# Performance work log

Measured on AMD Instinct MI355X. Metric: run time of the kernel, lower is better.

The kernel has to match this reference:

```python
import jax, jax.numpy as jnp
import numpy as np

B, C, H, W = 4, 256, 48, 48
KD, NH, AR = 32, 8, 4
D = AR * KD            # 128, value dim per head
NHKD = NH * KD         # 256
DH = NH * D            # 1024
EPS = 1e-5


def _bn(y, g, b):
    # BN with fresh running stats (mean=0, var=1): y*g/sqrt(1+eps)+b, over channel dim
    s = g / jnp.sqrt(jnp.float32(1.0) + EPS)
    return y * s[None, :, None] + b[None, :, None]


def setup_inputs() -> dict:
    key = jax.random.key(0)
    ks = jax.random.split(key, 13)
    w = lambda k, sh: jax.random.normal(k, sh, jnp.float32) * 0.05
    g = lambda k, sh: 1.0 + jax.random.normal(k, sh, jnp.float32) * 0.05
    return {
        "x": jax.random.normal(ks[0], (B, C, H, W), jnp.float32),
        "wq": w(ks[1], (NHKD, C)), "gq": g(ks[2], (NHKD,)), "bq": w(ks[3], (NHKD,)),
        "wk": w(ks[4], (NHKD, C)), "gk": g(ks[5], (NHKD,)), "bk": w(ks[6], (NHKD,)),
        "wv": w(ks[7], (DH, C)),   "gv": g(ks[8], (DH,)),   "bv": w(ks[9], (DH,)),
        "wp": w(ks[10], (C, DH)),  "gp": g(ks[11], (C,)),   "bp": w(ks[12], (C,)),
    }


def reference(x, wq, gq, bq, wk, gk, bk, wv, gv, bv, wp, gp, bp):
    b, c, h, w = x.shape
    n = h * w
    xf = x.reshape(b, c, n)                                   # [B,C,N]
    # 1x1 conv == channel matmul, then BN
    q = _bn(jnp.einsum('oc,bcn->bon', wq, xf), gq, bq).reshape(b, NH, KD, n)
    k = _bn(jnp.einsum('oc,bcn->bon', wk, xf), gk, bk).reshape(b, NH, KD, n)
    v = _bn(jnp.einsum('oc,bcn->bon', wv, xf), gv, bv).reshape(b, NH, D, n)
    # NOTE: original forward does NOT apply self.scale
    attn = jax.nn.softmax(jnp.einsum('bhkn,bhkm->bhnm', q, k), axis=-1)  # [B,H,N,N]
    xx = jnp.einsum('bhnm,bhdm->bhdn', attn, v).reshape(b, DH, n)        # [B,DH,N]
    out = _bn(jnp.einsum('oc,bcn->bon', wp, jax.nn.relu(xx)), gp, bp)
    return out.reshape(b, c, h, w)
```

## Files before the change

### kernel.cpp

```cpp
#include <hip/hip_runtime.h>

#define BB 4
#define C 256
#define HW 2304
#define NH 8
#define KD 32
#define D 128
#define DH 1024
#define MQ 256

typedef unsigned short bf16u;
typedef __attribute__((ext_vector_type(8))) short short8;
typedef __attribute__((ext_vector_type(4))) short bfx4;
typedef __attribute__((ext_vector_type(4))) float f32x4;
typedef __attribute__((ext_vector_type(4))) unsigned ux4;
typedef __attribute__((ext_vector_type(2))) unsigned ux2;

union U8 { ux4 u; short8 s; };

__device__ __forceinline__ bf16u f2b(float f) {
    unsigned u = __float_as_uint(f);
    return (bf16u)((u + 0x7fffu + ((u >> 16) & 1u)) >> 16);
}
__device__ __forceinline__ unsigned pkb(float a, float b) {
    return __builtin_amdgcn_perm(__float_as_uint(b) + 0x8000u,
                                 __float_as_uint(a) + 0x8000u, 0x07060302u);
}

__device__ __forceinline__ void glds16(const bf16u* g, bf16u* l) {
    __builtin_amdgcn_global_load_lds(
        (const __attribute__((address_space(1))) unsigned int*)g,
        (__attribute__((address_space(3))) unsigned int*)l,
        16, 0, 0);
}

#define MFMA32 __builtin_amdgcn_mfma_f32_16x16x32_bf16

__global__ __launch_bounds__(256) void prep(
    const float* __restrict__ wq, const float* __restrict__ wk, const float* __restrict__ wv,
    const float* __restrict__ gq, const float* __restrict__ bq,
    const float* __restrict__ gk, const float* __restrict__ bk,
    const float* __restrict__ gv, const float* __restrict__ bv,
    bf16u* __restrict__ WcT, float* __restrict__ biasc)
{
    const float rs = rsqrtf(1.0f + 1e-5f);
    const float L2E = 1.4426950408889634f;
    const int t = threadIdx.x, blk = blockIdx.x;
    if (blk < 192) {
        const int idx = (blk*256 + t) * 8;
        const int row = idx >> 8;
        const int k   = idx & 255;
        const float* src; float sc;
        if (row < 256)      { src = wq + idx;            sc = gq[row]*rs*L2E; }
        else if (row < 512) { src = wk + (idx - 65536);  sc = gk[row-256]*rs; }
        else                { src = wv + (idx - 131072); sc = gv[row-512]*rs; }
        float4 a = *(const float4*)(src);
        float4 c = *(const float4*)(src + 4);
        ux4 v;
        v.x = pkb(a.x*sc, a.y*sc); v.y = pkb(a.z*sc, a.w*sc);
        v.z = pkb(c.x*sc, c.y*sc); v.w = pkb(c.z*sc, c.w*sc);
        const size_t dst = (size_t)((row>>7)*8 + (k>>5))*4096
                         + (size_t)((row&127)*4 + ((k&31)>>3))*8;
        *(ux4*)(WcT + dst) = v;
    } else {
        #pragma unroll
        for (int kk = 0; kk < 6; ++kk) {
            const int r = kk*256 + t;
            float v;
            if (r < 256)      v = bq[r] * L2E;
            else if (r < 512) v = bk[r - 256];
            else              v = bv[r - 512];
            biasc[r] = v;
        }
    }
}

__global__ __launch_bounds__(256) void xtrans(const float* __restrict__ x,
                                              bf16u* __restrict__ xT)
{
    const int c0 = blockIdx.x * 64, n0 = blockIdx.y * 64, b = blockIdx.z;
    const int t = threadIdx.x;
    __shared__ float tile[64][68];

    const float* xb = x + (size_t)b * C * HW;
    #pragma unroll
    for (int rr = 0; rr < 4; ++rr) {
        const int cl = rr*16 + (t >> 4);
        float4 v = *(const float4*)(xb + (size_t)(c0 + cl) * HW + n0 + (t & 15)*4);
        tile[cl][(t&15)*4+0] = v.x; tile[cl][(t&15)*4+1] = v.y;
        tile[cl][(t&15)*4+2] = v.z; tile[cl][(t&15)*4+3] = v.w;
    }
    __syncthreads();
    const int nl = t >> 2, ch = t & 3;
    short8 v0, v1;
    #pragma unroll
    for (int kk = 0; kk < 8; ++kk) v0[kk] = (short)f2b(tile[ch*16+kk][nl]);
    #pragma unroll
    for (int kk = 0; kk < 8; ++kk) v1[kk] = (short)f2b(tile[ch*16+8+kk][nl]);
    bf16u* dst = xT + ((size_t)b*HW + n0 + nl) * C + c0 + ch*16;
    *(short8*)(dst)     = v0;
    *(short8*)(dst + 8) = v1;
}

__global__ __launch_bounds__(256, 3) void qkv_gemm(
    const bf16u* __restrict__ WcT, const float* __restrict__ biasc,
    const bf16u* __restrict__ xT,
    bf16u* __restrict__ qT, bf16u* __restrict__ kT, bf16u* __restrict__ vO)
{
    const int mt = blockIdx.x, ntb = blockIdx.y, b = blockIdx.z;
    const int r0 = mt * 128, c0 = ntb * 128;
    const int t = threadIdx.x, w = t >> 6, l = t & 63;
    const int l15 = l & 15, q = l >> 4;
    const int wr = w >> 1, wc = w & 1;

    __shared__ bf16u smem[24576];

    const bf16u* xb = xT + (size_t)b * HW * C;

    const int sA0 = w*128 + l, sA1 = w*128 + 64 + l;
    const bf16u* gA0 = WcT + (size_t)mt*32768 + (size_t)sA0*8;
    const bf16u* gA1 = WcT + (size_t)mt*32768 + (size_t)sA1*8;
    const bf16u* gB0 = xb + (size_t)(c0 + (sA0>>2)) * C + (sA0&3)*8;
    const bf16u* gB1 = xb + (size_t)(c0 + (sA1>>2)) * C + (sA1&3)*8;

    f32x4 acc[4][4];
    #pragma unroll
    for (int i = 0; i < 4; ++i)
        #pragma unroll
        for (int j = 0; j < 4; ++j) { acc[i][j][0]=0.f; acc[i][j][1]=0.f; acc[i][j][2]=0.f; acc[i][j][3]=0.f; }

    auto stage = [&](int it2, int bb) {
        bf16u* As = smem + bb*4096;
        bf16u* Bs = smem + 12288 + bb*4096;
        glds16(gA0 + it2*4096, As + sA0*8);
        glds16(gA1 + it2*4096, As + sA1*8);
        glds16(gB0 + it2*32,   Bs + sA0*8);
        glds16(gB1 + it2*32,   Bs + sA1*8);
    };

    const bool isV = (r0 >= 512);
    stage(0, 0); stage(1, 1);
    for (int it = 0; it < 8; ++it) {
        __syncthreads();
        if (it + 2 < 8) stage(it + 2, (it + 2) % 3);
        const bf16u* A = smem + (it % 3) * 4096;
        const bf16u* B = smem + 12288 + (it % 3) * 4096;
        short8 af[4], bf[4];
        #pragma unroll
        for (int i = 0; i < 4; ++i) af[i] = *(const short8*)(A + (wr*64 + i*16 + l15)*32 + q*8);
        #pragma unroll
        for (int j = 0; j < 4; ++j) bf[j] = *(const short8*)(B + (wc*64 + j*16 + l15)*32 + q*8);
        if (!isV) {
            #pragma unroll
            for (int i = 0; i < 4; ++i)
                #pragma unroll
                for (int j = 0; j < 4; ++j)
                    acc[i][j] = MFMA32(af[i], bf[j], acc[i][j], 0, 0, 0);
        } else {
            #pragma unroll
            for (int i = 0; i < 4; ++i)
                #pragma unroll
                for (int j = 0; j < 4; ++j)
                    acc[i][j] = MFMA32(bf[j], af[i], acc[i][j], 0, 0, 0);
        }
    }

    __syncthreads();
    bf16u* Od = smem + w * 4608;

    if (!isV) {
        float bC[4][4];
        #pragma unroll
        for (int i = 0; i < 4; ++i)
            #pragma unroll
            for (int r = 0; r < 4; ++r)
                bC[i][r] = biasc[r0 + wr*64 + i*16 + q*4 + r];
        #pragma unroll
        for (int i = 0; i < 4; ++i)
            #pragma unroll
            for (int j = 0; j < 4; ++j) {
                float y0 = acc[i][j][0] + bC[i][0];
                float y1 = acc[i][j][1] + bC[i][1];
                float y2 = acc[i][j][2] + bC[i][2];
                float y3 = acc[i][j][3] + bC[i][3];
                ux2 pk; pk.x = pkb(y0, y1); pk.y = pkb(y2, y3);
                *(ux2*)(Od + (j*16 + l15)*72 + i*16 + q*4) = pk;
            }
        bf16u* dst = (r0 < 256) ? qT : kT;
        #pragma unroll
        for (int hh = 0; hh < 2; ++hh) {
            const int h = ((r0 & 255) + wr*64 + hh*32) >> 5;
            bf16u* dh_ = dst + (size_t)(b*NH + h) * HW * KD;
            #pragma unroll
            for (int rg = 0; rg < 4; ++rg) {
                const int row = rg*16 + (l >> 2);
                const int n = c0 + wc*64 + row;
                short8 v = *(const short8*)(Od + row*72 + hh*32 + (l & 3)*8);
                *(short8*)(dh_ + (size_t)n * KD + (l & 3)*8) = v;
            }
        }
    } else {
        float bC[4];
        #pragma unroll
        for (int i = 0; i < 4; ++i)
            bC[i] = biasc[r0 + wr*64 + i*16 + l15];
        #pragma unroll
        for (int i = 0; i < 4; ++i)
            #pragma unroll
            for (int j = 0; j < 4; ++j) {
                float y0 = acc[i][j][0] + bC[i];
                float y1 = acc[i][j][1] + bC[i];
                float y2 = acc[i][j][2] + bC[i];
                float y3 = acc[i][j][3] + bC[i];
                ux2 pk; pk.x = pkb(y0, y1); pk.y = pkb(y2, y3);
                const int p = (j >> 1)*32 + q*8 + (j & 1)*4;
                *(ux2*)(Od + (i*16 + l15)*72 + p) = pk;
            }
        bf16u* dst = vO + (size_t)b * DH * HW;
        #pragma unroll
        for (int it2 = 0; it2 < 8; ++it2) {
            const int row = it2*8 + (l >> 3);
            const int d = (r0 - 512) + wr*64 + row;
            short8 v = *(const short8*)(Od + row*72 + (l & 7)*8);
            *(short8*)(dst + (size_t)d * HW + c0 + wc*64 + (l & 7)*8) = v;
        }
    }
}

__global__ __launch_bounds__(256, 3) void attn_mfma(
    const bf16u* __restrict__ qT, const bf16u* __restrict__ kT,
    const bf16u* __restrict__ vg, bf16u* __restrict__ xg)
{
    const int nt = blockIdx.x, h = blockIdx.y, b = blockIdx.z;
    const int n0 = nt * 128;
    const int t = threadIdx.x;
    const int w = t >> 6, l = t & 63, l15 = l & 15, q = l >> 4;

    const bf16u* qTh = qT + (size_t)(b*NH + h) * HW * KD;
    const bf16u* kTh = kT + (size_t)(b*NH + h) * HW * KD;
    const bf16u* vh  = vg + ((size_t)b*DH + (size_t)h*D) * HW;

    __shared__ bf16u smem[17408];

    short8 qf0 = *(const short8*)(qTh + (size_t)(n0 + w*32 +      l15) * KD + q*8);
    short8 qf1 = *(const short8*)(qTh + (size_t)(n0 + w*32 + 16 + l15) * KD + q*8);

    f32x4 o[2][8];
    #pragma unroll
    for (int a = 0; a < 2; ++a)
        #pragma unroll
        for (int d = 0; d < 8; ++d) { o[a][d][0]=0.f; o[a][d][1]=0.f; o[a][d][2]=0.f; o[a][d][3]=0.f; }
    float psum0 = 0.f, psum1 = 0.f;
    const f32x4 zero = {0.f, 0.f, 0.f, 0.f};

    auto stageV = [&](int m0, int bb) {
        bf16u* Vs = smem + bb*8192;
        #pragma unroll
        for (int j = 0; j < 4; ++j) {
            const int s = (w*4 + j)*64 + l;
            const int d = s >> 3, c = s & 7, cg = c ^ (d & 7);
            glds16(vh + (size_t)d*HW + m0 + cg*8, Vs + (w*4 + j)*512);
        }
    };

    short8 kfc[4], kfn[4];
    #pragma unroll
    for (int kt = 0; kt < 4; ++kt)
        kfc[kt] = *(const short8*)(kTh + (size_t)(kt*16 + l15) * KD + q*8);
    stageV(0, 0);

    for (int mt = 0; mt < 36; ++mt) {
        __syncthreads();
        if (mt < 35) {
            stageV((mt+1)*64, (mt+1)&1);
            #pragma unroll
            for (int kt = 0; kt < 4; ++kt)
                kfn[kt] = *(const short8*)(kTh + (size_t)((mt+1)*64 + kt*16 + l15) * KD + q*8);
        }
        const bf16u* Vs = smem + (mt&1)*8192;

        f32x4 st0[4], st1[4];
        #pragma unroll
        for (int kt = 0; kt < 4; ++kt) {
            st0[kt] = MFMA32(kfc[kt], qf0, zero, 0, 0, 0);
            st1[kt] = MFMA32(kfc[kt], qf1, zero, 0, 0, 0);
        }

        unsigned dA0[4], dB0[4], dA1[4], dB1[4];
        #pragma unroll
        for (int kt = 0; kt < 4; ++kt) {
            float p0 = __builtin_amdgcn_exp2f(st0[kt][0]);
            float p1 = __builtin_amdgcn_exp2f(st0[kt][1]);
            float p2 = __builtin_amdgcn_exp2f(st0[kt][2]);
            float p3 = __builtin_amdgcn_exp2f(st0[kt][3]);
            psum0 += (p0 + p1) + (p2 + p3);
            dA0[kt] = pkb(p0, p1); dB0[kt] = pkb(p2, p3);
            float r0_ = __builtin_amdgcn_exp2f(st1[kt][0]);
            float r1_ = __builtin_amdgcn_exp2f(st1[kt][1]);
            float r2_ = __builtin_amdgcn_exp2f(st1[kt][2]);
            float r3_ = __builtin_amdgcn_exp2f(st1[kt][3]);
            psum1 += (r0_ + r1_) + (r2_ + r3_);
            dA1[kt] = pkb(r0_, r1_); dB1[kt] = pkb(r2_, r3_);
        }

        #pragma unroll
        for (int kh = 0; kh < 2; ++kh) {
            U8 u0, u1;
            u0.u[0] = dA0[kh*2];   u0.u[1] = dB0[kh*2];
            u0.u[2] = dA0[kh*2+1]; u0.u[3] = dB0[kh*2+1];
            u1.u[0] = dA1[kh*2];   u1.u[1] = dB1[kh*2];
            u1.u[2] = dA1[kh*2+1]; u1.u[3] = dB1[kh*2+1];
            #pragma unroll
            for (int dt = 0; dt < 8; ++dt) {
                const int d = dt*16 + l15;
                short8 vf = *(const short8*)(Vs + d*64 + (((kh*4 + q) ^ (d & 7)) * 8));
                o[0][dt] = MFMA32(u0.s, vf, o[0][dt], 0, 0, 0);
                o[1][dt] = MFMA32(u1.s, vf, o[1][dt], 0, 0, 0);
            }
        }

        if (mt < 35) {
            #pragma unroll
            for (int kt = 0; kt < 4; ++kt) kfc[kt] = kfn[kt];
        }
    }

    psum0 += __shfl_xor(psum0, 16); psum0 += __shfl_xor(psum0, 32);
    psum1 += __shfl_xor(psum1, 16); psum1 += __shfl_xor(psum1, 32);
    float inv0[4], inv1[4];
    #pragma unroll
    for (int r = 0; r < 4; ++r) {
        inv0[r] = 1.0f / __shfl(psum0, q*4 + r);
        inv1[r] = 1.0f / __shfl(psum1, q*4 + r);
    }
    __syncthreads();
    bf16u* Od = smem + w * 4352;
    #pragma unroll
    for (int dt = 0; dt < 8; ++dt)
        #pragma unroll
        for (int r = 0; r < 4; ++r) {
            float v0 = fmaxf(o[0][dt][r] * inv0[r], 0.f);
            float v1 = fmaxf(o[1][dt][r] * inv1[r], 0.f);
            Od[(     q*4 + r)*136 + dt*16 + l15] = f2b(v0);
            Od[(16 + q*4 + r)*136 + dt*16 + l15] = f2b(v1);
        }
    bf16u* xb = xg + ((size_t)b*HW + n0 + w*32) * DH + h*D;
    #pragma unroll
    for (int g = 0; g < 4; ++g) {
        const int row = g*8 + (l >> 3);
        #pragma unroll
        for (int hf = 0; hf < 2; ++hf) {
            const int ch = hf*8 + (l & 7);
            *(short8*)(xb + (size_t)row*DH + ch*8) =
                *(const short8*)(Od + row*136 + ch*8);
        }
    }
}

__global__ __launch_bounds__(256) void prep2(
    const float* __restrict__ wp, const float* __restrict__ gp,
    bf16u* __restrict__ WpT)
{
    const float rs = rsqrtf(1.0f + 1e-5f);
    const int item = blockIdx.x*256 + threadIdx.x;
    const int row = item >> 7;
    const int k   = (item & 127) * 8;
    const float sc = gp[row] * rs;
    const float* src = wp + (size_t)row*DH + k;
    float4 a = *(const float4*)(src);
    float4 c = *(const float4*)(src + 4);
    ux4 v;
    v.x = pkb(a.x*sc, a.y*sc); v.y = pkb(a.z*sc, a.w*sc);
    v.z = pkb(c.x*sc, c.y*sc); v.w = pkb(c.z*sc, c.w*sc);
    const size_t dst = (size_t)((row>>6)*16 + (k>>6))*4096
                     + (size_t)((row&63)*8 + ((k&63)>>3))*8;
    *(ux4*)(WpT + dst) = v;
}

__global__ __launch_bounds__(256, 3) void out_gemm(
    const bf16u* __restrict__ WpT, const float* __restrict__ bp,
    const bf16u* __restrict__ xx, float* __restrict__ out)
{
    const int mt = blockIdx.x, ntb = blockIdx.y, b = blockIdx.z;
    const int r0 = mt * 64, c0 = ntb * 64;
    const int t = threadIdx.x, w = t >> 6, l = t & 63;
    const int l15 = l & 15, q = l >> 4;
    const int wr = w >> 1, wc = w & 1;

    __shared__ bf16u smem[24576];

    const bf16u* xb = xx + (size_t)b * HW * DH;

    const int sA0 = t, sA1 = 256 + t;
    const bf16u* gA0 = WpT + (size_t)mt*65536 + (size_t)sA0*8;
    const bf16u* gA1 = WpT + (size_t)mt*65536 + (size_t)sA1*8;
    const int sB0 = w*128 + l, sB1 = w*128 + 64 + l;
    const bf16u* gB0 = xb + (size_t)(c0 + (sB0>>3)) * DH + (sB0&7)*8;
    const bf16u* gB1 = xb + (size_t)(c0 + (sB1>>3)) * DH + (sB1&7)*8;

    f32x4 acc[2][2];
    #pragma unroll
    for (int i = 0; i < 2; ++i)
        #pragma unroll
        for (int j = 0; j < 2; ++j) { acc[i][j][0]=0.f; acc[i][j][1]=0.f; acc[i][j][2]=0.f; acc[i][j][3]=0.f; }

    auto stage = [&](int it2, int bb) {
        bf16u* As = smem + bb*4096;
        bf16u* Bs = smem + 12288 + bb*4096;
        glds16(gA0 + it2*4096, As + sA0*8);
        glds16(gA1 + it2*4096, As + sA1*8);
        glds16(gB0 + it2*64,   Bs + sB0*8);
        glds16(gB1 + it2*64,   Bs + sB1*8);
    };

    stage(0, 0); stage(1, 1);
    for (int it = 0; it < 16; ++it) {
        __syncthreads();
        if (it + 2 < 16) stage(it + 2, (it + 2) % 3);
        const bf16u* A = smem + (it % 3) * 4096;
        const bf16u* B = smem + 12288 + (it % 3) * 4096;
        #pragma unroll
        for (int kk = 0; kk < 2; ++kk) {
            short8 af[2], bf[2];
            #pragma unroll
            for (int i = 0; i < 2; ++i) af[i] = *(const short8*)(A + (wr*32 + i*16 + l15)*64 + kk*32 + q*8);
            #pragma unroll
            for (int j = 0; j < 2; ++j) bf[j] = *(const short8*)(B + (wc*32 + j*16 + l15)*64 + kk*32 + q*8);
            #pragma unroll
            for (int i = 0; i < 2; ++i)
                #pragma unroll
                for (int j = 0; j < 2; ++j)
                    acc[i][j] = MFMA32(af[i], bf[j], acc[i][j], 0, 0, 0);
        }
    }

    #pragma unroll
    for (int i = 0; i < 2; ++i)
        #pragma unroll
        for (int r = 0; r < 4; ++r) {
            const int oc = r0 + wr*32 + i*16 + q*4 + r;
            const float bi = bp[oc];
            #pragma unroll
            for (int j = 0; j < 2; ++j) {
                const int n = c0 + wc*32 + j*16 + l15;
                out[((size_t)b*C + oc)*HW + n] = acc[i][j][r] + bi;
            }
        }
}

extern "C" void kernel_launch(void* const* d_in, const int* in_sizes, int n_in,
                              void* d_out, int out_size, void* d_ws, size_t ws_size,
                              hipStream_t stream) {
    const float* x  = (const float*)d_in[0];
    const float* wq = (const float*)d_in[1];
    const float* gq = (const float*)d_in[2];
    const float* bq = (const float*)d_in[3];
    const float* wk = (const float*)d_in[4];
    const float* gk = (const float*)d_in[5];
    const float* bk = (const float*)d_in[6];
    const float* wv = (const float*)d_in[7];
    const float* gv = (const float*)d_in[8];
    const float* bv = (const float*)d_in[9];
    const float* wp = (const float*)d_in[10];
    const float* gp = (const float*)d_in[11];
    const float* bp = (const float*)d_in[12];
    float* out = (float*)d_out;

    bf16u* qw = (bf16u*)d_ws;
    bf16u* kw = qw + (size_t)BB * MQ * HW;
    bf16u* vw = kw + (size_t)BB * MQ * HW;
    bf16u* xw = vw + (size_t)BB * DH * HW;
    bf16u* xTb = xw;
    bf16u* WcT = xw + (size_t)BB * MQ * HW;
    float* biasc = (float*)(WcT + 393216);
    bf16u* WpT = qw;

    hipLaunchKernelGGL(prep, dim3(193), dim3(256), 0, stream,
                       wq, wk, wv, gq, bq, gk, bk, gv, bv, WcT, biasc);
    hipLaunchKernelGGL(xtrans, dim3(4, 36, BB), dim3(256), 0, stream, x, xTb);
    hipLaunchKernelGGL(qkv_gemm, dim3(12, 18, BB), dim3(256), 0, stream,
                       WcT, biasc, xTb, qw, kw, vw);
    hipLaunchKernelGGL(attn_mfma, dim3(18, NH, BB), dim3(256), 0, stream,
                       qw, kw, vw, xw);
    hipLaunchKernelGGL(prep2, dim3(128), dim3(256), 0, stream, wp, gp, WpT);
    hipLaunchKernelGGL(out_gemm, dim3(4, 36, BB), dim3(256), 0, stream,
                       WpT, bp, xw, out);
}
```

Baseline: 199.2 us.

## Merge prep with x transpose and split attention blocks across value dim

```diff
diff --git a/kernel.cpp b/kernel.cpp
--- a/kernel.cpp
+++ b/kernel.cpp
@@ -36,13 +36,15 @@
 
 #define MFMA32 __builtin_amdgcn_mfma_f32_16x16x32_bf16
 
-__global__ __launch_bounds__(256) void prep(
+__global__ __launch_bounds__(256) void prepx(
     const float* __restrict__ wq, const float* __restrict__ wk, const float* __restrict__ wv,
     const float* __restrict__ gq, const float* __restrict__ bq,
     const float* __restrict__ gk, const float* __restrict__ bk,
     const float* __restrict__ gv, const float* __restrict__ bv,
-    bf16u* __restrict__ WcT, float* __restrict__ biasc)
+    const float* __restrict__ x,
+    bf16u* __restrict__ WcT, float* __restrict__ biasc, bf16u* __restrict__ xT)
 {
+    __shared__ float tile[64][68];
     const float rs = rsqrtf(1.0f + 1e-5f);
     const float L2E = 1.4426950408889634f;
     const int t = threadIdx.x, blk = blockIdx.x;
@@ -62,7 +64,7 @@
         const size_t dst = (size_t)((row>>7)*8 + (k>>5))*4096
                          + (size_t)((row&127)*4 + ((k&31)>>3))*8;
         *(ux4*)(WcT + dst) = v;
-    } else {
+    } else if (blk == 192) {
         #pragma unroll
         for (int kk = 0; kk < 6; ++kk) {
             const int r = kk*256 + t;
@@ -72,34 +74,28 @@
             else              v = bv[r - 512];
             biasc[r] = v;
         }
-    }
-}
-
-__global__ __launch_bounds__(256) void xtrans(const float* __restrict__ x,
-                                              bf16u* __restrict__ xT)
-{
-    const int c0 = blockIdx.x * 64, n0 = blockIdx.y * 64, b = blockIdx.z;
-    const int t = threadIdx.x;
-    __shared__ float tile[64][68];
-
-    const float* xb = x + (size_t)b * C * HW;
-    #pragma unroll
-    for (int rr = 0; rr < 4; ++rr) {
-        const int cl = rr*16 + (t >> 4);
-        float4 v = *(const float4*)(xb + (size_t)(c0 + cl) * HW + n0 + (t & 15)*4);
-        tile[cl][(t&15)*4+0] = v.x; tile[cl][(t&15)*4+1] = v.y;
-        tile[cl][(t&15)*4+2] = v.z; tile[cl][(t&15)*4+3] = v.w;
-    }
-    __syncthreads();
-    const int nl = t >> 2, ch = t & 3;
-    short8 v0, v1;
-    #pragma unroll
-    for (int kk = 0; kk < 8; ++kk) v0[kk] = (short)f2b(tile[ch*16+kk][nl]);
-    #pragma unroll
-    for (int kk = 0; kk < 8; ++kk) v1[kk] = (short)f2b(tile[ch*16+8+kk][nl]);
-    bf16u* dst = xT + ((size_t)b*HW + n0 + nl) * C + c0 + ch*16;
-    *(short8*)(dst)     = v0;
-    *(short8*)(dst + 8) = v1;
+    } else {
+        const int idx = blk - 193;
+        const int c0 = (idx & 3) * 64, n0 = ((idx >> 2) % 36) * 64, b = idx / 144;
+        const float* xb = x + (size_t)b * C * HW;
+        #pragma unroll
+        for (int rr = 0; rr < 4; ++rr) {
+            const int cl = rr*16 + (t >> 4);
+            float4 v = *(const float4*)(xb + (size_t)(c0 + cl) * HW + n0 + (t & 15)*4);
+            tile[cl][(t&15)*4+0] = v.x; tile[cl][(t&15)*4+1] = v.y;
+            tile[cl][(t&15)*4+2] = v.z; tile[cl][(t&15)*4+3] = v.w;
+        }
+        __syncthreads();
+        const int nl = t >> 2, ch = t & 3;
+        short8 v0, v1;
+        #pragma unroll
+        for (int kk = 0; kk < 8; ++kk) v0[kk] = (short)f2b(tile[ch*16+kk][nl]);
+        #pragma unroll
+        for (int kk = 0; kk < 8; ++kk) v1[kk] = (short)f2b(tile[ch*16+8+kk][nl]);
+        bf16u* dst = xT + ((size_t)b*HW + n0 + nl) * C + c0 + ch*16;
+        *(short8*)(dst)     = v0;
+        *(short8*)(dst + 8) = v1;
+    }
 }
 
 __global__ __launch_bounds__(256, 3) void qkv_gemm(
@@ -227,29 +223,30 @@
     }
 }
 
-__global__ __launch_bounds__(256, 3) void attn_mfma(
+__global__ __launch_bounds__(256, 4) void attn_mfma(
     const bf16u* __restrict__ qT, const bf16u* __restrict__ kT,
     const bf16u* __restrict__ vg, bf16u* __restrict__ xg)
 {
     const int nt = blockIdx.x, h = blockIdx.y, b = blockIdx.z;
-    const int n0 = nt * 128;
+    const int n0 = nt * 64;
     const int t = threadIdx.x;
     const int w = t >> 6, l = t & 63, l15 = l & 15, q = l >> 4;
+    const int qh = w >> 1, dh = w & 1;
 
     const bf16u* qTh = qT + (size_t)(b*NH + h) * HW * KD;
     const bf16u* kTh = kT + (size_t)(b*NH + h) * HW * KD;
     const bf16u* vh  = vg + ((size_t)b*DH + (size_t)h*D) * HW;
 
-    __shared__ bf16u smem[17408];
-
-    short8 qf0 = *(const short8*)(qTh + (size_t)(n0 + w*32 +      l15) * KD + q*8);
-    short8 qf1 = *(const short8*)(qTh + (size_t)(n0 + w*32 + 16 + l15) * KD + q*8);
-
-    f32x4 o[2][8];
+    __shared__ bf16u smem[16384];
+
+    short8 qf0 = *(const short8*)(qTh + (size_t)(n0 + qh*32 +      l15) * KD + q*8);
+    short8 qf1 = *(const short8*)(qTh + (size_t)(n0 + qh*32 + 16 + l15) * KD + q*8);
+
+    f32x4 o[2][4];
     #pragma unroll
     for (int a = 0; a < 2; ++a)
         #pragma unroll
-        for (int d = 0; d < 8; ++d) { o[a][d][0]=0.f; o[a][d][1]=0.f; o[a][d][2]=0.f; o[a][d][3]=0.f; }
+        for (int d = 0; d < 4; ++d) { o[a][d][0]=0.f; o[a][d][1]=0.f; o[a][d][2]=0.f; o[a][d][3]=0.f; }
     float psum0 = 0.f, psum1 = 0.f;
     const f32x4 zero = {0.f, 0.f, 0.f, 0.f};
 
@@ -311,8 +308,8 @@
             u1.u[0] = dA1[kh*2];   u1.u[1] = dB1[kh*2];
             u1.u[2] = dA1[kh*2+1]; u1.u[3] = dB1[kh*2+1];
             #pragma unroll
-            for (int dt = 0; dt < 8; ++dt) {
-                const int d = dt*16 + l15;
+            for (int dt = 0; dt < 4; ++dt) {
+                const int d = dh*64 + dt*16 + l15;
                 short8 vf = *(const short8*)(Vs + d*64 + (((kh*4 + q) ^ (d & 7)) * 8));
                 o[0][dt] = MFMA32(u0.s, vf, o[0][dt], 0, 0, 0);
                 o[1][dt] = MFMA32(u1.s, vf, o[1][dt], 0, 0, 0);
@@ -334,26 +331,22 @@
         inv1[r] = 1.0f / __shfl(psum1, q*4 + r);
     }
     __syncthreads();
-    bf16u* Od = smem + w * 4352;
-    #pragma unroll
-    for (int dt = 0; dt < 8; ++dt)
+    bf16u* Od = smem + w * 2304;
+    #pragma unroll
+    for (int dt = 0; dt < 4; ++dt)
         #pragma unroll
         for (int r = 0; r < 4; ++r) {
             float v0 = fmaxf(o[0][dt][r] * inv0[r], 0.f);
             float v1 = fmaxf(o[1][dt][r] * inv1[r], 0.f);
-            Od[(     q*4 + r)*136 + dt*16 + l15] = f2b(v0);
-            Od[(16 + q*4 + r)*136 + dt*16 + l15] = f2b(v1);
-        }
-    bf16u* xb = xg + ((size_t)b*HW + n0 + w*32) * DH + h*D;
+            Od[(     q*4 + r)*72 + dt*16 + l15] = f2b(v0);
+            Od[(16 + q*4 + r)*72 + dt*16 + l15] = f2b(v1);
+        }
+    bf16u* xb = xg + ((size_t)b*HW + n0 + qh*32) * DH + h*D + dh*64;
     #pragma unroll
     for (int g = 0; g < 4; ++g) {
         const int row = g*8 + (l >> 3);
-        #pragma unroll
-        for (int hf = 0; hf < 2; ++hf) {
-            const int ch = hf*8 + (l & 7);
-            *(short8*)(xb + (size_t)row*DH + ch*8) =
-                *(const short8*)(Od + row*136 + ch*8);
-        }
+        *(short8*)(xb + (size_t)row*DH + (l & 7)*8) =
+            *(const short8*)(Od + row*72 + (l & 7)*8);
     }
 }
 
@@ -475,12 +468,11 @@
     float* biasc = (float*)(WcT + 393216);
     bf16u* WpT = qw;
 
-    hipLaunchKernelGGL(prep, dim3(193), dim3(256), 0, stream,
-                       wq, wk, wv, gq, bq, gk, bk, gv, bv, WcT, biasc);
-    hipLaunchKernelGGL(xtrans, dim3(4, 36, BB), dim3(256), 0, stream, x, xTb);
+    hipLaunchKernelGGL(prepx, dim3(769), dim3(256), 0, stream,
+                       wq, wk, wv, gq, bq, gk, bk, gv, bv, x, WcT, biasc, xTb);
     hipLaunchKernelGGL(qkv_gemm, dim3(12, 18, BB), dim3(256), 0, stream,
                        WcT, biasc, xTb, qw, kw, vw);
-    hipLaunchKernelGGL(attn_mfma, dim3(18, NH, BB), dim3(256), 0, stream,
+    hipLaunchKernelGGL(attn_mfma, dim3(36, NH, BB), dim3(256), 0, stream,
                        qw, kw, vw, xw);
     hipLaunchKernelGGL(prep2, dim3(128), dim3(256), 0, stream, wp, gp, WpT);
     hipLaunchKernelGGL(out_gemm, dim3(4, 36, BB), dim3(256), 0, stream,
```

New measurement: 217.1 us. +9.0%, slower.
